# Kernel tuning notes

Measured on AMD Instinct MI355X. Metric: run time of the kernel, lower is better.

The kernel has to match this reference:

```python
import jax, jax.numpy as jnp
import numpy as np

H = 32

def setup_inputs() -> dict:
    key = jax.random.key(0)
    ks = jax.random.split(key, 8)
    B, S = 256, 4096
    scale = 1.0 / np.sqrt(H)
    return {
        "lstm_outputs": jax.random.normal(ks[0], (B, S, H), dtype=jnp.float32),
        "final_hidden": jax.random.normal(ks[1], (B, H), dtype=jnp.float32),
        "Wq": jax.random.uniform(ks[2], (H, H), jnp.float32, -scale, scale),
        "bq": jax.random.uniform(ks[3], (H,), jnp.float32, -scale, scale),
        "Wk": jax.random.uniform(ks[4], (H, H), jnp.float32, -scale, scale),
        "bk": jax.random.uniform(ks[5], (H,), jnp.float32, -scale, scale),
        "Wv": jax.random.uniform(ks[6], (H, 1), jnp.float32, -scale, scale),
        "bv": jax.random.uniform(ks[7], (1,), jnp.float32, -scale, scale),
    }

def reference(lstm_outputs, final_hidden, Wq, bq, Wk, bk, Wv, bv):
    # keys: [B,S,H], query: [B,H]
    keys = jnp.einsum('bsh,hd->bsd', lstm_outputs, Wk) + bk
    query = final_hidden @ Wq + bq
    tanhed = jnp.tanh(query[:, None, :] + keys)            # [B,S,H]
    scores = jnp.einsum('bsh,h->bs', tanhed, Wv[:, 0]) + bv[0]  # [B,S]
    att_weights = jax.nn.softmax(scores, axis=-1)          # [B,S]
    context = jnp.einsum('bs,bsh->bh', att_weights, keys)  # [B,H]
    return context, att_weights
```

## Files before the change

### kernel.cpp

```cpp
#include <hip/hip_runtime.h>
#include <math.h>

#define HD 32
#define BB 256
#define SS 4096
#define BLK 256
#define POSB 256
#define NCH (SS / POSB)
#define NWREC 64
#define PREC 36

typedef short bf16x8 __attribute__((ext_vector_type(8)));
typedef float f32x4 __attribute__((ext_vector_type(4)));

__device__ __forceinline__ float tanh_fast(float x) {
  float e = __builtin_amdgcn_exp2f(x * 2.8853900817779268f);
  return 1.0f - 2.0f * __builtin_amdgcn_rcpf(e + 1.0f);
}
__device__ __forceinline__ float exp_fast(float x) {
  return __builtin_amdgcn_exp2f(x * 1.4426950408889634f);
}
__device__ __forceinline__ short bf16_trunc(float x) {
  return (short)(__float_as_uint(x) >> 16);
}
__device__ __forceinline__ float hi_part(float x) {
  return __uint_as_float(__float_as_uint(x) & 0xffff0000u);
}

__global__ void __launch_bounds__(256) bahdanau_p0(
    const float* __restrict__ fh, const float* __restrict__ Wq,
    const float* __restrict__ bq, const float* __restrict__ bk,
    const float* __restrict__ Wk, float* __restrict__ qbP,
    short* __restrict__ wkH, short* __restrict__ wkL) {
  const int tid = threadIdx.x;
  if (blockIdx.x == 32) {
    float4 w4 = ((const float4*)Wk)[tid];
    const int k = tid >> 3, h0 = (tid & 7) * 4;
    const float v[4] = {w4.x, w4.y, w4.z, w4.w};
#pragma unroll
    for (int i = 0; i < 4; i++) {
      const float hf = hi_part(v[i]);
      wkH[(h0 + i) * HD + k] = bf16_trunc(v[i]);
      wkL[(h0 + i) * HD + k] = bf16_trunc(v[i] - hf);
    }
  } else {
    const int b = blockIdx.x * 8 + (tid >> 5);
    const int h = tid & 31;
    float acc = bq[h] + bk[h];
    const float* fhb = fh + b * HD;
#pragma unroll
    for (int j = 0; j < HD; j++) acc = fmaf(fhb[j], Wq[j * HD + h], acc);
    qbP[b * HD + h] = acc;
  }
}

__global__ void __launch_bounds__(BLK, 4) bahdanau_p1(
    const float* __restrict__ lstm, const float* __restrict__ qbP,
    const short* __restrict__ wkH, const short* __restrict__ wkL,
    const float* __restrict__ Wv, const float* __restrict__ bv,
    float* __restrict__ scores_out, float* __restrict__ partials) {
  const int tid = threadIdx.x;
  const int b = blockIdx.x >> 4;
  const int chunk = blockIdx.x & (NCH - 1);
  const int base = chunk * POSB;
  const int lane = tid & 63, w = tid >> 6;
  const int col = lane & 15, quad = lane >> 4;

  const float* rp =
      lstm + ((size_t)b * SS + base + w * 64 + col) * HD + quad * 8;
  float4 xa0 = ((const float4*)(rp + 0 * 16 * HD))[0];
  float4 xb0 = ((const float4*)(rp + 0 * 16 * HD))[1];
  float4 xa1 = ((const float4*)(rp + 1 * 16 * HD))[0];
  float4 xb1 = ((const float4*)(rp + 1 * 16 * HD))[1];
  float4 xa2 = ((const float4*)(rp + 2 * 16 * HD))[0];
  float4 xb2 = ((const float4*)(rp + 2 * 16 * HD))[1];
  float4 xa3 = ((const float4*)(rp + 3 * 16 * HD))[0];
  float4 xb3 = ((const float4*)(rp + 3 * 16 * HD))[1];

  const bf16x8 Ah0 = *(const bf16x8*)&wkH[col * HD + quad * 8];
  const bf16x8 Al0 = *(const bf16x8*)&wkL[col * HD + quad * 8];
  const bf16x8 Ah1 = *(const bf16x8*)&wkH[(16 + col) * HD + quad * 8];
  const bf16x8 Al1 = *(const bf16x8*)&wkL[(16 + col) * HD + quad * 8];
  const float4 qbA = ((const float4*)(qbP + b * HD))[quad];
  const float4 qbB = ((const float4*)(qbP + b * HD))[quad + 4];
  const float4 wvA = ((const float4*)Wv)[quad];
  const float4 wvB = ((const float4*)Wv)[quad + 4];
  const float bv0 = bv[0];

  float lAcc = 0.f;
  float yp[8];
#pragma unroll
  for (int j = 0; j < 8; j++) yp[j] = 0.f;

  const size_t srow = (size_t)b * SS + base;

#define MT_STEP(mt, XA, XB)                                                    \
  {                                                                            \
    const float xs[8] = {XA.x, XA.y, XA.z, XA.w, XB.x, XB.y, XB.z, XB.w};      \
    bf16x8 Bh, Bl;                                                             \
    _Pragma("unroll") for (int j = 0; j < 8; j++) {                            \
      const float hf = hi_part(xs[j]);                                         \
      Bh[j] = bf16_trunc(xs[j]);                                               \
      Bl[j] = bf16_trunc(xs[j] - hf);                                          \
    }                                                                          \
    f32x4 c0 = {0.f, 0.f, 0.f, 0.f}, c1 = {0.f, 0.f, 0.f, 0.f};                \
    c0 = __builtin_amdgcn_mfma_f32_16x16x32_bf16(Ah0, Bh, c0, 0, 0, 0);        \
    c1 = __builtin_amdgcn_mfma_f32_16x16x32_bf16(Ah1, Bh, c1, 0, 0, 0);        \
    c0 = __builtin_amdgcn_mfma_f32_16x16x32_bf16(Al0, Bh, c0, 0, 0, 0);        \
    c1 = __builtin_amdgcn_mfma_f32_16x16x32_bf16(Al1, Bh, c1, 0, 0, 0);        \
    c0 = __builtin_amdgcn_mfma_f32_16x16x32_bf16(Ah0, Bl, c0, 0, 0, 0);        \
    c1 = __builtin_amdgcn_mfma_f32_16x16x32_bf16(Ah1, Bl, c1, 0, 0, 0);        \
    float t = tanh_fast(c0[0] + qbA.x) * wvA.x;                                \
    t = fmaf(tanh_fast(c0[1] + qbA.y), wvA.y, t);                              \
    t = fmaf(tanh_fast(c0[2] + qbA.z), wvA.z, t);                              \
    t = fmaf(tanh_fast(c0[3] + qbA.w), wvA.w, t);                              \
    t = fmaf(tanh_fast(c1[0] + qbB.x), wvB.x, t);                              \
    t = fmaf(tanh_fast(c1[1] + qbB.y), wvB.y, t);                              \
    t = fmaf(tanh_fast(c1[2] + qbB.z), wvB.z, t);                              \
    t = fmaf(tanh_fast(c1[3] + qbB.w), wvB.w, t);                              \
    t += __shfl_xor(t, 16, 64);                                                \
    t += __shfl_xor(t, 32, 64);                                                \
    const float e_m = exp_fast(t + bv0);     \
    if (lane < 16) scores_out[srow + w * 64 + mt * 16 + lane] = e_m;           \
    lAcc += (lane < 16) ? e_m : 0.f;                                           \
    _Pragma("unroll") for (int j = 0; j < 8; j++)                              \
        yp[j] = fmaf(e_m, xs[j], yp[j]);                                       \
  }

  MT_STEP(0, xa0, xb0)
  MT_STEP(1, xa1, xb1)
  MT_STEP(2, xa2, xb2)
  MT_STEP(3, xa3, xb3)
#undef MT_STEP

#pragma unroll
  for (int j = 0; j < 8; j++) {
    yp[j] += __shfl_xor(yp[j], 1, 64);
    yp[j] += __shfl_xor(yp[j], 2, 64);
    yp[j] += __shfl_xor(yp[j], 4, 64);
    yp[j] += __shfl_xor(yp[j], 8, 64);
  }
  lAcc += __shfl_xor(lAcc, 1, 64);
  lAcc += __shfl_xor(lAcc, 2, 64);
  lAcc += __shfl_xor(lAcc, 4, 64);
  lAcc += __shfl_xor(lAcc, 8, 64);

  float* rec = partials + (size_t)(blockIdx.x * 4 + w) * PREC;
  if (col == 0) {
    const float4 y0 = {yp[0], yp[1], yp[2], yp[3]};
    const float4 y1 = {yp[4], yp[5], yp[6], yp[7]};
    ((float4*)(rec + 4))[quad * 2] = y0;
    ((float4*)(rec + 4))[quad * 2 + 1] = y1;
  }
  if (lane == 0) rec[0] = lAcc;
}

__global__ void __launch_bounds__(BLK) bahdanau_p2(
    const float* __restrict__ partials, const float* __restrict__ Wk,
    const float* __restrict__ bk, float* __restrict__ ctx_out,
    float* __restrict__ scores) {
  const int blk = blockIdx.x;
  const int b = blk >> 2;
  const int tid = threadIdx.x;
  __shared__ float sY[HD];

  float L = 0.f;
#pragma unroll 8
  for (int c = 0; c < NWREC; c++)
    L += partials[(size_t)(b * NWREC + c) * PREC];
  const float invL = __builtin_amdgcn_rcpf(L);

  if ((blk & 3) == 0) {
    if (tid < HD) {
      float y = 0.f;
#pragma unroll 8
      for (int c = 0; c < NWREC; c++)
        y += partials[(size_t)(b * NWREC + c) * PREC + 4 + tid];
      sY[tid] = y;
    }
    __syncthreads();
    if (tid < HD) {
      float cv = bk[tid] * L;
#pragma unroll
      for (int j = 0; j < HD; j++) cv = fmaf(sY[j], Wk[j * HD + tid], cv);
      ctx_out[b * HD + tid] = cv * invL;
    }
  }

  float4* srow = (float4*)(scores + (size_t)b * SS + (blk & 3) * 1024);
  float4 s = srow[tid];
  s.x *= invL; s.y *= invL; s.z *= invL; s.w *= invL;
  srow[tid] = s;
}

extern "C" void kernel_launch(void* const* d_in, const int* in_sizes, int n_in,
                              void* d_out, int out_size, void* d_ws,
                              size_t ws_size, hipStream_t stream) {
  const float* lstm = (const float*)d_in[0];
  const float* fh   = (const float*)d_in[1];
  const float* Wq   = (const float*)d_in[2];
  const float* bq   = (const float*)d_in[3];
  const float* Wk   = (const float*)d_in[4];
  const float* bk   = (const float*)d_in[5];
  const float* Wv   = (const float*)d_in[6];
  const float* bv   = (const float*)d_in[7];

  float* out = (float*)d_out;
  float* ctx_out = out;
  float* scores = out + BB * HD;

  float* partials = (float*)d_ws;
  short* wkH = (short*)((char*)d_ws + (size_t)BB * NWREC * PREC * 4);
  short* wkL = wkH + HD * HD;
  float* qbP = (float*)(wkL + HD * HD);

  bahdanau_p0<<<33, 256, 0, stream>>>(fh, Wq, bq, bk, Wk, qbP, wkH, wkL);
  bahdanau_p1<<<BB * NCH, BLK, 0, stream>>>(lstm, qbP, wkH, wkL, Wv, bv,
                                            scores, partials);
  bahdanau_p2<<<BB * 4, BLK, 0, stream>>>(partials, Wk, bk, ctx_out, scores);
}
```

Baseline: 211.4 us.

## Process four position chunks per block with double-buffered register prefetch

Each p1 block now handles four 256-position chunks instead of one, so the grid drops from 4096 to 1024 blocks. Loads for the next chunk are issued into a second register set while the current chunk is computed. The tanh-weighted sum is also rebalanced into a tree of independent adds to shorten the dependency chain. Fewer partial records (16 per batch row) shrink p2's reduction loop, but the extra live registers and lower block count may reduce occupancy and latency hiding.

```diff
diff --git a/kernel.cpp b/kernel.cpp
--- a/kernel.cpp
+++ b/kernel.cpp
@@ -6,8 +6,8 @@
 #define SS 4096
 #define BLK 256
 #define POSB 256
-#define NCH (SS / POSB)
-#define NWREC 64
+#define GRP 4
+#define NWREC 16
 #define PREC 36
 
 typedef short bf16x8 __attribute__((ext_vector_type(8)));
@@ -60,22 +60,32 @@
     const float* __restrict__ Wv, const float* __restrict__ bv,
     float* __restrict__ scores_out, float* __restrict__ partials) {
   const int tid = threadIdx.x;
-  const int b = blockIdx.x >> 4;
-  const int chunk = blockIdx.x & (NCH - 1);
-  const int base = chunk * POSB;
+  const int b = blockIdx.x >> 2;
+  const int grp = blockIdx.x & 3;
+  const int base = grp * (GRP * POSB);
   const int lane = tid & 63, w = tid >> 6;
   const int col = lane & 15, quad = lane >> 4;
 
   const float* rp =
       lstm + ((size_t)b * SS + base + w * 64 + col) * HD + quad * 8;
-  float4 xa0 = ((const float4*)(rp + 0 * 16 * HD))[0];
-  float4 xb0 = ((const float4*)(rp + 0 * 16 * HD))[1];
-  float4 xa1 = ((const float4*)(rp + 1 * 16 * HD))[0];
-  float4 xb1 = ((const float4*)(rp + 1 * 16 * HD))[1];
-  float4 xa2 = ((const float4*)(rp + 2 * 16 * HD))[0];
-  float4 xb2 = ((const float4*)(rp + 2 * 16 * HD))[1];
-  float4 xa3 = ((const float4*)(rp + 3 * 16 * HD))[0];
-  float4 xb3 = ((const float4*)(rp + 3 * 16 * HD))[1];
+
+  float4 pa0, pb0, pa1, pb1, pa2, pb2, pa3, pb3;
+  float4 qa0, qb0_, qa1, qb1_, qa2, qb2_, qa3, qb3_;
+
+#define LOADC(cc, A0, B0, A1, B1, A2, B2, A3, B3)                              \
+  {                                                                            \
+    const float* p_ = rp + (size_t)(cc) * (POSB * HD);                         \
+    A0 = ((const float4*)(p_ + 0 * 16 * HD))[0];                               \
+    B0 = ((const float4*)(p_ + 0 * 16 * HD))[1];                               \
+    A1 = ((const float4*)(p_ + 1 * 16 * HD))[0];                               \
+    B1 = ((const float4*)(p_ + 1 * 16 * HD))[1];                               \
+    A2 = ((const float4*)(p_ + 2 * 16 * HD))[0];                               \
+    B2 = ((const float4*)(p_ + 2 * 16 * HD))[1];                               \
+    A3 = ((const float4*)(p_ + 3 * 16 * HD))[0];                               \
+    B3 = ((const float4*)(p_ + 3 * 16 * HD))[1];                               \
+  }
+
+  LOADC(0, pa0, pb0, pa1, pb1, pa2, pb2, pa3, pb3)
 
   const bf16x8 Ah0 = *(const bf16x8*)&wkH[col * HD + quad * 8];
   const bf16x8 Al0 = *(const bf16x8*)&wkL[col * HD + quad * 8];
@@ -94,7 +104,7 @@
 
   const size_t srow = (size_t)b * SS + base;
 
-#define MT_STEP(mt, XA, XB)                                                    \
+#define MT_STEP(cc, mt, XA, XB)                                                \
   {                                                                            \
     const float xs[8] = {XA.x, XA.y, XA.z, XA.w, XB.x, XB.y, XB.z, XB.w};      \
     bf16x8 Bh, Bl;                                                             \
@@ -110,28 +120,41 @@
     c1 = __builtin_amdgcn_mfma_f32_16x16x32_bf16(Al1, Bh, c1, 0, 0, 0);        \
     c0 = __builtin_amdgcn_mfma_f32_16x16x32_bf16(Ah0, Bl, c0, 0, 0, 0);        \
     c1 = __builtin_amdgcn_mfma_f32_16x16x32_bf16(Ah1, Bl, c1, 0, 0, 0);        \
-    float t = tanh_fast(c0[0] + qbA.x) * wvA.x;                                \
-    t = fmaf(tanh_fast(c0[1] + qbA.y), wvA.y, t);                              \
-    t = fmaf(tanh_fast(c0[2] + qbA.z), wvA.z, t);                              \
-    t = fmaf(tanh_fast(c0[3] + qbA.w), wvA.w, t);                              \
-    t = fmaf(tanh_fast(c1[0] + qbB.x), wvB.x, t);                              \
-    t = fmaf(tanh_fast(c1[1] + qbB.y), wvB.y, t);                              \
-    t = fmaf(tanh_fast(c1[2] + qbB.z), wvB.z, t);                              \
-    t = fmaf(tanh_fast(c1[3] + qbB.w), wvB.w, t);                              \
+    const float t0 = tanh_fast(c0[0] + qbA.x) * wvA.x;                         \
+    const float t1 = tanh_fast(c0[1] + qbA.y) * wvA.y;                         \
+    const float t2 = tanh_fast(c0[2] + qbA.z) * wvA.z;                         \
+    const float t3 = tanh_fast(c0[3] + qbA.w) * wvA.w;                         \
+    const float t4 = tanh_fast(c1[0] + qbB.x) * wvB.x;                         \
+    const float t5 = tanh_fast(c1[1] + qbB.y) * wvB.y;                         \
+    const float t6 = tanh_fast(c1[2] + qbB.z) * wvB.z;                         \
+    const float t7 = tanh_fast(c1[3] + qbB.w) * wvB.w;                         \
+    float t = ((t0 + t1) + (t2 + t3)) + ((t4 + t5) + (t6 + t7));               \
     t += __shfl_xor(t, 16, 64);                                                \
     t += __shfl_xor(t, 32, 64);                                                \
     const float e_m = exp_fast(t + bv0);     \
-    if (lane < 16) scores_out[srow + w * 64 + mt * 16 + lane] = e_m;           \
+    if (lane < 16)                                                             \
+      scores_out[srow + (cc)*POSB + w * 64 + (mt)*16 + lane] = e_m;            \
     lAcc += (lane < 16) ? e_m : 0.f;                                           \
     _Pragma("unroll") for (int j = 0; j < 8; j++)                              \
         yp[j] = fmaf(e_m, xs[j], yp[j]);                                       \
   }
 
-  MT_STEP(0, xa0, xb0)
-  MT_STEP(1, xa1, xb1)
-  MT_STEP(2, xa2, xb2)
-  MT_STEP(3, xa3, xb3)
+#define CHUNK(cc, A0, B0, A1, B1, A2, B2, A3, B3)                              \
+  MT_STEP(cc, 0, A0, B0)                                                       \
+  MT_STEP(cc, 1, A1, B1)                                                       \
+  MT_STEP(cc, 2, A2, B2)                                                       \
+  MT_STEP(cc, 3, A3, B3)
+
+  LOADC(1, qa0, qb0_, qa1, qb1_, qa2, qb2_, qa3, qb3_)
+  CHUNK(0, pa0, pb0, pa1, pb1, pa2, pb2, pa3, pb3)
+  LOADC(2, pa0, pb0, pa1, pb1, pa2, pb2, pa3, pb3)
+  CHUNK(1, qa0, qb0_, qa1, qb1_, qa2, qb2_, qa3, qb3_)
+  LOADC(3, qa0, qb0_, qa1, qb1_, qa2, qb2_, qa3, qb3_)
+  CHUNK(2, pa0, pb0, pa1, pb1, pa2, pb2, pa3, pb3)
+  CHUNK(3, qa0, qb0_, qa1, qb1_, qa2, qb2_, qa3, qb3_)
+#undef CHUNK
 #undef MT_STEP
+#undef LOADC
 
 #pragma unroll
   for (int j = 0; j < 8; j++) {
@@ -165,7 +188,7 @@
   __shared__ float sY[HD];
 
   float L = 0.f;
-#pragma unroll 8
+#pragma unroll
   for (int c = 0; c < NWREC; c++)
     L += partials[(size_t)(b * NWREC + c) * PREC];
   const float invL = __builtin_amdgcn_rcpf(L);
@@ -173,7 +196,7 @@
   if ((blk & 3) == 0) {
     if (tid < HD) {
       float y = 0.f;
-#pragma unroll 8
+#pragma unroll
       for (int c = 0; c < NWREC; c++)
         y += partials[(size_t)(b * NWREC + c) * PREC + 4 + tid];
       sY[tid] = y;
@@ -215,7 +238,7 @@
   float* qbP = (float*)(wkL + HD * HD);
 
   bahdanau_p0<<<33, 256, 0, stream>>>(fh, Wq, bq, bk, Wk, qbP, wkH, wkL);
-  bahdanau_p1<<<BB * NCH, BLK, 0, stream>>>(lstm, qbP, wkH, wkL, Wv, bv,
-                                            scores, partials);
+  bahdanau_p1<<<BB * 4, BLK, 0, stream>>>(lstm, qbP, wkH, wkL, Wv, bv,
+                                          scores, partials);
   bahdanau_p2<<<BB * 4, BLK, 0, stream>>>(partials, Wk, bk, ctx_out, scores);
 }
```

Measured after the change: 256.0 us. +21.1%, slower.

## Stage lstm rows through LDS with async global_load_lds triple buffering

Applied to the files above, without the earlier changes.

The main kernel now processes 512 positions per block instead of 256, halving the grid and the number of partial records. Input rows are fetched with asynchronous global-to-LDS loads into a swizzled triple buffer, and explicit vmcnt waits let MFMA/tanh work on one stage overlap with loads of the next. Score stores are deferred to the end, and the tanh reduction becomes a tree. The cost is 48KB of LDS per block, which lowers occupancy (launch bounds reduced to 3), and hand-written wait counts that must match the issued loads exactly.

```diff
diff --git a/kernel.cpp b/kernel.cpp
--- a/kernel.cpp
+++ b/kernel.cpp
@@ -5,9 +5,7 @@
 #define BB 256
 #define SS 4096
 #define BLK 256
-#define POSB 256
-#define NCH (SS / POSB)
-#define NWREC 64
+#define NWREC 32
 #define PREC 36
 
 typedef short bf16x8 __attribute__((ext_vector_type(8)));
@@ -54,28 +52,17 @@
   }
 }
 
-__global__ void __launch_bounds__(BLK, 4) bahdanau_p1(
+__global__ void __launch_bounds__(BLK, 3) bahdanau_p1(
     const float* __restrict__ lstm, const float* __restrict__ qbP,
     const short* __restrict__ wkH, const short* __restrict__ wkL,
     const float* __restrict__ Wv, const float* __restrict__ bv,
     float* __restrict__ scores_out, float* __restrict__ partials) {
+  __shared__ __align__(16) float sX[4 * 3 * 1024];
   const int tid = threadIdx.x;
-  const int b = blockIdx.x >> 4;
-  const int chunk = blockIdx.x & (NCH - 1);
-  const int base = chunk * POSB;
+  const int b = blockIdx.x >> 3;
+  const int grp = blockIdx.x & 7;
   const int lane = tid & 63, w = tid >> 6;
   const int col = lane & 15, quad = lane >> 4;
-
-  const float* rp =
-      lstm + ((size_t)b * SS + base + w * 64 + col) * HD + quad * 8;
-  float4 xa0 = ((const float4*)(rp + 0 * 16 * HD))[0];
-  float4 xb0 = ((const float4*)(rp + 0 * 16 * HD))[1];
-  float4 xa1 = ((const float4*)(rp + 1 * 16 * HD))[0];
-  float4 xb1 = ((const float4*)(rp + 1 * 16 * HD))[1];
-  float4 xa2 = ((const float4*)(rp + 2 * 16 * HD))[0];
-  float4 xb2 = ((const float4*)(rp + 2 * 16 * HD))[1];
-  float4 xa3 = ((const float4*)(rp + 3 * 16 * HD))[0];
-  float4 xb3 = ((const float4*)(rp + 3 * 16 * HD))[1];
 
   const bf16x8 Ah0 = *(const bf16x8*)&wkH[col * HD + quad * 8];
   const bf16x8 Al0 = *(const bf16x8*)&wkL[col * HD + quad * 8];
@@ -87,15 +74,37 @@
   const float4 wvB = ((const float4*)Wv)[quad + 4];
   const float bv0 = bv[0];
 
+  char* wlds = (char*)sX + w * 12288;
+  const char* gw =
+      (const char*)(lstm + ((size_t)b * SS + grp * 512 + w * 128) * HD) +
+      ((lane ^ ((lane >> 3) & 7)) << 4);
+  const int rOff0 = (col * 128 + quad * 32) ^ ((col & 7) << 4);
+
+#define STAGE(t, buf)                                                          \
+  {                                                                            \
+    _Pragma("unroll") for (int i = 0; i < 4; i++)                              \
+        __builtin_amdgcn_global_load_lds(                                      \
+            (const __attribute__((address_space(1))) void*)(gw + (t)*4096 +    \
+                                                            i * 1024),         \
+            (__attribute__((address_space(3))) void*)(wlds + (buf)*4096 +      \
+                                                      i * 1024),               \
+            16, 0, 0);                                                         \
+  }
+#define WAITV(n)                                                               \
+  asm volatile("s_waitcnt vmcnt(" #n ")" ::: "memory");                        \
+  __builtin_amdgcn_sched_barrier(0);
+
   float lAcc = 0.f;
   float yp[8];
 #pragma unroll
   for (int j = 0; j < 8; j++) yp[j] = 0.f;
-
-  const size_t srow = (size_t)b * SS + base;
-
-#define MT_STEP(mt, XA, XB)                                                    \
+  float e0, e1, e2, e3, e4, e5, e6, e7;
+
+#define MT_STEP(buf, s, EOUT)                                                  \
   {                                                                            \
+    const char* pr_ = wlds + (buf)*4096 + (s)*2048;                            \
+    const float4 XA = *(const float4*)(pr_ + rOff0);                           \
+    const float4 XB = *(const float4*)(pr_ + (rOff0 ^ 16));                    \
     const float xs[8] = {XA.x, XA.y, XA.z, XA.w, XB.x, XB.y, XB.z, XB.w};      \
     bf16x8 Bh, Bl;                                                             \
     _Pragma("unroll") for (int j = 0; j < 8; j++) {                            \
@@ -110,28 +119,49 @@
     c1 = __builtin_amdgcn_mfma_f32_16x16x32_bf16(Al1, Bh, c1, 0, 0, 0);        \
     c0 = __builtin_amdgcn_mfma_f32_16x16x32_bf16(Ah0, Bl, c0, 0, 0, 0);        \
     c1 = __builtin_amdgcn_mfma_f32_16x16x32_bf16(Ah1, Bl, c1, 0, 0, 0);        \
-    float t = tanh_fast(c0[0] + qbA.x) * wvA.x;                                \
-    t = fmaf(tanh_fast(c0[1] + qbA.y), wvA.y, t);                              \
-    t = fmaf(tanh_fast(c0[2] + qbA.z), wvA.z, t);                              \
-    t = fmaf(tanh_fast(c0[3] + qbA.w), wvA.w, t);                              \
-    t = fmaf(tanh_fast(c1[0] + qbB.x), wvB.x, t);                              \
-    t = fmaf(tanh_fast(c1[1] + qbB.y), wvB.y, t);                              \
-    t = fmaf(tanh_fast(c1[2] + qbB.z), wvB.z, t);                              \
-    t = fmaf(tanh_fast(c1[3] + qbB.w), wvB.w, t);                              \
+    const float t0 = tanh_fast(c0[0] + qbA.x) * wvA.x;                         \
+    const float t1 = tanh_fast(c0[1] + qbA.y) * wvA.y;                         \
+    const float t2 = tanh_fast(c0[2] + qbA.z) * wvA.z;                         \
+    const float t3 = tanh_fast(c0[3] + qbA.w) * wvA.w;                         \
+    const float t4 = tanh_fast(c1[0] + qbB.x) * wvB.x;                         \
+    const float t5 = tanh_fast(c1[1] + qbB.y) * wvB.y;                         \
+    const float t6 = tanh_fast(c1[2] + qbB.z) * wvB.z;                         \
+    const float t7 = tanh_fast(c1[3] + qbB.w) * wvB.w;                         \
+    float t = ((t0 + t1) + (t2 + t3)) + ((t4 + t5) + (t6 + t7));               \
     t += __shfl_xor(t, 16, 64);                                                \
     t += __shfl_xor(t, 32, 64);                                                \
     const float e_m = exp_fast(t + bv0);     \
-    if (lane < 16) scores_out[srow + w * 64 + mt * 16 + lane] = e_m;           \
+    EOUT = e_m;                                                                \
     lAcc += (lane < 16) ? e_m : 0.f;                                           \
     _Pragma("unroll") for (int j = 0; j < 8; j++)                              \
         yp[j] = fmaf(e_m, xs[j], yp[j]);                                       \
   }
 
-  MT_STEP(0, xa0, xb0)
-  MT_STEP(1, xa1, xb1)
-  MT_STEP(2, xa2, xb2)
-  MT_STEP(3, xa3, xb3)
+  STAGE(0, 0)
+  STAGE(1, 1)
+  STAGE(2, 2)
+  WAITV(8)
+  MT_STEP(0, 0, e0)
+  MT_STEP(0, 1, e1)
+  STAGE(3, 0)
+  WAITV(8)
+  MT_STEP(1, 0, e2)
+  MT_STEP(1, 1, e3)
+  WAITV(4)
+  MT_STEP(2, 0, e4)
+  MT_STEP(2, 1, e5)
+  WAITV(0)
+  MT_STEP(0, 0, e6)
+  MT_STEP(0, 1, e7)
 #undef MT_STEP
+#undef STAGE
+#undef WAITV
+
+  if (lane < 16) {
+    float* sp = scores_out + (size_t)b * SS + grp * 512 + w * 128 + lane;
+    sp[0] = e0;  sp[16] = e1;  sp[32] = e2;  sp[48] = e3;
+    sp[64] = e4; sp[80] = e5;  sp[96] = e6;  sp[112] = e7;
+  }
 
 #pragma unroll
   for (int j = 0; j < 8; j++) {
@@ -215,7 +245,7 @@
   float* qbP = (float*)(wkL + HD * HD);
 
   bahdanau_p0<<<33, 256, 0, stream>>>(fh, Wq, bq, bk, Wk, qbP, wkH, wkL);
-  bahdanau_p1<<<BB * NCH, BLK, 0, stream>>>(lstm, qbP, wkH, wkL, Wv, bv,
-                                            scores, partials);
+  bahdanau_p1<<<BB * 8, BLK, 0, stream>>>(lstm, qbP, wkH, wkL, Wv, bv,
+                                          scores, partials);
   bahdanau_p2<<<BB * 4, BLK, 0, stream>>>(partials, Wk, bk, ctx_out, scores);
 }
```

Result: no change. 209.2 us (-1.0%).

## Halve per-block positions and reduce warp partials in shared memory

Applied to the files above, without the earlier changes.

Each p1 block now covers 128 sequence positions instead of 256, two MFMA tiles per wave instead of four, and the grid doubles to 8192 blocks. The launch-bounds occupancy hint rises from 4 to 5. Per-wave partial sums are combined in shared memory so each block writes one partial record, which keeps p2's record count at 32 per batch row. The goal is more blocks and fewer live registers for better latency hiding on the memory-bound read. The cost is a block barrier, more per-block setup loads of the weights, and more blocks to schedule.

```diff
diff --git a/kernel.cpp b/kernel.cpp
--- a/kernel.cpp
+++ b/kernel.cpp
@@ -5,9 +5,7 @@
 #define BB 256
 #define SS 4096
 #define BLK 256
-#define POSB 256
-#define NCH (SS / POSB)
-#define NWREC 64
+#define NWREC 32
 #define PREC 36
 
 typedef short bf16x8 __attribute__((ext_vector_type(8)));
@@ -54,28 +52,25 @@
   }
 }
 
-__global__ void __launch_bounds__(BLK, 4) bahdanau_p1(
+__global__ void __launch_bounds__(BLK, 5) bahdanau_p1(
     const float* __restrict__ lstm, const float* __restrict__ qbP,
     const short* __restrict__ wkH, const short* __restrict__ wkL,
     const float* __restrict__ Wv, const float* __restrict__ bv,
     float* __restrict__ scores_out, float* __restrict__ partials) {
+  __shared__ float sYp[4][HD];
+  __shared__ float sRedL[4];
   const int tid = threadIdx.x;
-  const int b = blockIdx.x >> 4;
-  const int chunk = blockIdx.x & (NCH - 1);
-  const int base = chunk * POSB;
+  const int b = blockIdx.x >> 5;
+  const int seg = blockIdx.x & 31;
   const int lane = tid & 63, w = tid >> 6;
   const int col = lane & 15, quad = lane >> 4;
 
   const float* rp =
-      lstm + ((size_t)b * SS + base + w * 64 + col) * HD + quad * 8;
-  float4 xa0 = ((const float4*)(rp + 0 * 16 * HD))[0];
-  float4 xb0 = ((const float4*)(rp + 0 * 16 * HD))[1];
-  float4 xa1 = ((const float4*)(rp + 1 * 16 * HD))[0];
-  float4 xb1 = ((const float4*)(rp + 1 * 16 * HD))[1];
-  float4 xa2 = ((const float4*)(rp + 2 * 16 * HD))[0];
-  float4 xb2 = ((const float4*)(rp + 2 * 16 * HD))[1];
-  float4 xa3 = ((const float4*)(rp + 3 * 16 * HD))[0];
-  float4 xb3 = ((const float4*)(rp + 3 * 16 * HD))[1];
+      lstm + ((size_t)b * SS + seg * 128 + w * 32 + col) * HD + quad * 8;
+  const float4 xa0 = ((const float4*)(rp + 0 * 16 * HD))[0];
+  const float4 xb0 = ((const float4*)(rp + 0 * 16 * HD))[1];
+  const float4 xa1 = ((const float4*)(rp + 1 * 16 * HD))[0];
+  const float4 xb1 = ((const float4*)(rp + 1 * 16 * HD))[1];
 
   const bf16x8 Ah0 = *(const bf16x8*)&wkH[col * HD + quad * 8];
   const bf16x8 Al0 = *(const bf16x8*)&wkL[col * HD + quad * 8];
@@ -92,7 +87,7 @@
 #pragma unroll
   for (int j = 0; j < 8; j++) yp[j] = 0.f;
 
-  const size_t srow = (size_t)b * SS + base;
+  const size_t srow = (size_t)b * SS + seg * 128 + w * 32;
 
 #define MT_STEP(mt, XA, XB)                                                    \
   {                                                                            \
@@ -121,7 +116,7 @@
     t += __shfl_xor(t, 16, 64);                                                \
     t += __shfl_xor(t, 32, 64);                                                \
     const float e_m = exp_fast(t + bv0);     \
-    if (lane < 16) scores_out[srow + w * 64 + mt * 16 + lane] = e_m;           \
+    if (lane < 16) scores_out[srow + (mt)*16 + lane] = e_m;                    \
     lAcc += (lane < 16) ? e_m : 0.f;                                           \
     _Pragma("unroll") for (int j = 0; j < 8; j++)                              \
         yp[j] = fmaf(e_m, xs[j], yp[j]);                                       \
@@ -129,8 +124,6 @@
 
   MT_STEP(0, xa0, xb0)
   MT_STEP(1, xa1, xb1)
-  MT_STEP(2, xa2, xb2)
-  MT_STEP(3, xa3, xb3)
 #undef MT_STEP
 
 #pragma unroll
@@ -140,19 +133,21 @@
     yp[j] += __shfl_xor(yp[j], 4, 64);
     yp[j] += __shfl_xor(yp[j], 8, 64);
   }
-  lAcc += __shfl_xor(lAcc, 1, 64);
-  lAcc += __shfl_xor(lAcc, 2, 64);
-  lAcc += __shfl_xor(lAcc, 4, 64);
-  lAcc += __shfl_xor(lAcc, 8, 64);
-
-  float* rec = partials + (size_t)(blockIdx.x * 4 + w) * PREC;
+#pragma unroll
+  for (int off = 32; off >= 1; off >>= 1) lAcc += __shfl_xor(lAcc, off, 64);
+
   if (col == 0) {
-    const float4 y0 = {yp[0], yp[1], yp[2], yp[3]};
-    const float4 y1 = {yp[4], yp[5], yp[6], yp[7]};
-    ((float4*)(rec + 4))[quad * 2] = y0;
-    ((float4*)(rec + 4))[quad * 2 + 1] = y1;
-  }
-  if (lane == 0) rec[0] = lAcc;
+#pragma unroll
+    for (int j = 0; j < 8; j++) sYp[w][quad * 8 + j] = yp[j];
+  }
+  if (lane == 0) sRedL[w] = lAcc;
+  __syncthreads();
+
+  if (tid < HD) {
+    float* rec = partials + (size_t)blockIdx.x * PREC;
+    rec[4 + tid] = sYp[0][tid] + sYp[1][tid] + sYp[2][tid] + sYp[3][tid];
+    if (tid == 0) rec[0] = sRedL[0] + sRedL[1] + sRedL[2] + sRedL[3];
+  }
 }
 
 __global__ void __launch_bounds__(BLK) bahdanau_p2(
@@ -215,7 +210,7 @@
   float* qbP = (float*)(wkL + HD * HD);
 
   bahdanau_p0<<<33, 256, 0, stream>>>(fh, Wq, bq, bk, Wk, qbP, wkH, wkL);
-  bahdanau_p1<<<BB * NCH, BLK, 0, stream>>>(lstm, qbP, wkH, wkL, Wv, bv,
-                                            scores, partials);
+  bahdanau_p1<<<BB * 32, BLK, 0, stream>>>(lstm, qbP, wkH, wkL, Wv, bv,
+                                           scores, partials);
   bahdanau_p2<<<BB * 4, BLK, 0, stream>>>(partials, Wk, bk, ctx_out, scores);
 }
```

Result: faster. 206.9 us (median of 2 runs) (-2.1%).
